# Kernel tuning notes

Measured on AMD Instinct MI355X. Metric: run time of the kernel, lower is better.

Reference implementation:

```python
import jax, jax.numpy as jnp
import numpy as np


def reference(x, weight, bias):
    """Per-sample dynamic conv2d, expressed as one grouped convolution.

    x:      (B, C_in, H, W)
    weight: (B, C_out, C_in, kH, kW)
    bias:   (B, C_out)
    returns (B, C_out, H_out, W_out) with H_out = H - kH + 1 (valid conv)
    """
    B, C_in, H, W = x.shape
    C_out, kH, kW = weight.shape[1], weight.shape[3], weight.shape[4]
    # Fold batch into channels: groups=B grouped conv == B independent convs.
    x_g = x.reshape(1, B * C_in, H, W)
    w_g = weight.reshape(B * C_out, C_in, kH, kW)
    out = jax.lax.conv_general_dilated(
        x_g, w_g,
        window_strides=(1, 1),
        padding='VALID',
        dimension_numbers=('NCHW', 'OIHW', 'NCHW'),
        feature_group_count=B,
    )  # (1, B*C_out, H_out, W_out)
    out = out.reshape(B, C_out, out.shape[2], out.shape[3])
    return out + bias[:, :, None, None]


def setup_inputs() -> dict:
    key = jax.random.key(0)
    k1, k2, k3 = jax.random.split(key, 3)
    B, C_in, C_out, H, W, kH, kW = 16, 64, 64, 128, 128, 3, 3
    x = jax.random.normal(k1, (B, C_in, H, W), dtype=jnp.float32)
    weight = jax.random.normal(k2, (B, C_out, C_in, kH, kW), dtype=jnp.float32) * 0.05
    bias = jax.random.normal(k3, (B, C_out), dtype=jnp.float32)
    return {"x": x, "weight": weight, "bias": bias}
```

## Files before the change

kernel.cpp:

```cpp
#include <hip/hip_runtime.h>
#include <hip/hip_bf16.h>

#define BATCH 16
#define CI 64
#define CO 64
#define H 128
#define W 128
#define HO 126
#define WO 126
#define HW (H * W)

typedef short bfrag __attribute__((ext_vector_type(8)));
typedef float ffrag __attribute__((ext_vector_type(4)));

static __device__ __forceinline__ unsigned short f2bf(float f) {
    unsigned u = __float_as_uint(f);
    u += 0x7fffu + ((u >> 16) & 1u);
    return (unsigned short)(u >> 16);
}

__global__ void wt_prepass(const float* __restrict__ w, unsigned short* __restrict__ w_t) {
    int i = blockIdx.x * 256 + threadIdx.x;
    int ci = i & 63;
    int co = (i >> 6) & 63;
    int bs = i >> 12;
    int b = bs / 9, s = bs - b * 9;
    w_t[i] = f2bf(w[(((b * 64 + co) * 64 + ci) * 9) + s]);
}

static __device__ __forceinline__ void stage_write(unsigned short* __restrict__ slabp,
                                                   const float4* __restrict__ v,
                                                   int st_o, int st_cg) {
    #pragma unroll
    for (int k = 0; k < 4; ++k) {
        const int col = st_cg * 4 + k;
        unsigned int u[4];
        #pragma unroll
        for (int e = 0; e < 4; ++e) {
            __hip_bfloat162 h2 = __float22bfloat162_rn(make_float2(
                ((const float*)&v[2 * e])[k], ((const float*)&v[2 * e + 1])[k]));
            u[e] = *(unsigned int*)&h2;
        }
        *(uint4*)&slabp[(col * 8 + (st_o ^ (col & 7))) * 8] = *(const uint4*)u;
    }
}

__launch_bounds__(256, 2)
__global__ void dynconv_fused(const float* __restrict__ x,
                              const unsigned short* __restrict__ w_t,
                              const float* __restrict__ bias,
                              float* __restrict__ out) {
    __shared__ __align__(16) unsigned short xs[4 * 8192];

    const int tid = threadIdx.x;
    const int gx  = blockIdx.x;
    const int b   = blockIdx.y;
    const int y0  = gx * 4;
    const int nunits = (gx == 31) ? 2 : 4;

    const int wave = tid >> 6, lane = tid & 63;
    const int l16 = lane & 15, lq = lane >> 4;

    const int st_o  = tid & 7;
    const int st_cg = tid >> 3;

    const float* stp = x + (size_t)b * CI * HW + (size_t)(st_o * 8) * HW + st_cg * 4;

    const bfrag* wtb = (const bfrag*)w_t + (size_t)(b * 9) * 512;
    const int co_b = wave * 16 + l16;
    bfrag a[9][2];
    #pragma unroll
    for (int s = 0; s < 9; ++s)
        #pragma unroll
        for (int ks = 0; ks < 2; ++ks)
            a[s][ks] = wtb[s * 512 + co_b * 8 + ks * 4 + lq];

    float bv[4];
    #pragma unroll
    for (int r = 0; r < 4; ++r)
        bv[r] = bias[b * 64 + wave * 16 + lq * 4 + r];

    {
        float4 v[3][8];
        #pragma unroll
        for (int rr = 0; rr < 3; ++rr) {
            const float* p = stp + (size_t)(y0 + rr) * W;
            #pragma unroll
            for (int e = 0; e < 8; ++e) v[rr][e] = *(const float4*)(p + (size_t)e * HW);
        }
        #pragma unroll
        for (int rr = 0; rr < 3; ++rr)
            stage_write(&xs[rr * 8192], v[rr], st_o, st_cg);
    }
    asm volatile("s_waitcnt lgkmcnt(0)" ::: "memory");
    __builtin_amdgcn_s_barrier();
    __builtin_amdgcn_sched_barrier(0);

    for (int j = 0; j < nunits; ++j) {
        const bool hn = (j + 1) < nunits;

        float4 v[8];
        if (hn) {
            const float* p = stp + (size_t)(y0 + j + 3) * W;
            #pragma unroll
            for (int e = 0; e < 8; ++e) v[e] = *(const float4*)(p + (size_t)e * HW);
        }
        __builtin_amdgcn_sched_barrier(0);

        ffrag acc[8];
        #pragma unroll
        for (int nt = 0; nt < 8; ++nt) acc[nt] = (ffrag){0.f, 0.f, 0.f, 0.f};

        #pragma unroll
        for (int s = 0; s < 9; ++s) {
            const int dy = s / 3, dx = s - dy * 3;
            const unsigned short* slabp = &xs[((j + dy) & 3) * 8192];
            #pragma unroll
            for (int ks = 0; ks < 2; ++ks) {
                const int o = ks * 4 + lq;
                #pragma unroll
                for (int nt = 0; nt < 8; ++nt) {
                    int colx = nt * 16 + l16 + dx;
                    if (colx > 127) colx = 127;
                    const bfrag bf = *(const bfrag*)&slabp[(colx * 8 + (o ^ (colx & 7))) * 8];
                    acc[nt] = __builtin_amdgcn_mfma_f32_16x16x32_bf16(a[s][ks], bf, acc[nt], 0, 0, 0);
                }
            }
        }

        if (hn) {
            stage_write(&xs[((j + 3) & 3) * 8192], v, st_o, st_cg);
            asm volatile("s_waitcnt lgkmcnt(0)" ::: "memory");
            __builtin_amdgcn_s_barrier();
            __builtin_amdgcn_sched_barrier(0);
        }

        const int oy = y0 + j;
        #pragma unroll
        for (int r = 0; r < 4; ++r) {
            float* op = out + ((size_t)(b * 64 + wave * 16 + lq * 4 + r) * HO + oy) * WO;
            const float bvv = bv[r];
            #pragma unroll
            for (int nt = 0; nt < 8; ++nt) {
                const int ox = nt * 16 + l16;
                if (ox < WO) op[ox] = acc[nt][r] + bvv;
            }
        }
    }
}

extern "C" void kernel_launch(void* const* d_in, const int* in_sizes, int n_in,
                              void* d_out, int out_size, void* d_ws, size_t ws_size,
                              hipStream_t stream) {
    const float* x    = (const float*)d_in[0];
    const float* w    = (const float*)d_in[1];
    const float* bias = (const float*)d_in[2];
    float* out        = (float*)d_out;

    unsigned short* w_t = (unsigned short*)d_ws;

    wt_prepass<<<dim3(589824 / 256), dim3(256), 0, stream>>>(w, w_t);
    dynconv_fused<<<dim3(32, BATCH), dim3(256), 0, stream>>>(x, w_t, bias, out);
}
```

Before: 134.2 us.

## Deepen input row prefetch to two rows ahead with five-slot LDS ring

Prefetches input rows two units ahead into alternating register buffers (vA/vB) and grows the LDS ring from four to five slabs. The loop is manually unrolled by two so the register buffers swap roles. This gives global loads a full extra unit of compute to hide their latency. It costs more registers (16 float4 held live) and more LDS, 80KB per block, which could reduce occupancy below the two blocks per CU requested by launch bounds.

```diff
diff --git a/kernel.cpp b/kernel.cpp
--- a/kernel.cpp
+++ b/kernel.cpp
@@ -50,7 +50,7 @@
                               const unsigned short* __restrict__ w_t,
                               const float* __restrict__ bias,
                               float* __restrict__ out) {
-    __shared__ __align__(16) unsigned short xs[4 * 8192];
+    __shared__ __align__(16) unsigned short xs[5 * 8192];
 
     const int tid = threadIdx.x;
     const int gx  = blockIdx.x;
@@ -80,6 +80,8 @@
     for (int r = 0; r < 4; ++r)
         bv[r] = bias[b * 64 + wave * 16 + lq * 4 + r];
 
+    float4 vA[8], vB[8];
+
     {
         float4 v[3][8];
         #pragma unroll
@@ -87,6 +89,11 @@
             const float* p = stp + (size_t)(y0 + rr) * W;
             #pragma unroll
             for (int e = 0; e < 8; ++e) v[rr][e] = *(const float4*)(p + (size_t)e * HW);
+        }
+        {
+            const float* p = stp + (size_t)(y0 + 3) * W;
+            #pragma unroll
+            for (int e = 0; e < 8; ++e) vA[e] = *(const float4*)(p + (size_t)e * HW);
         }
         #pragma unroll
         for (int rr = 0; rr < 3; ++rr)
@@ -96,57 +103,55 @@
     __builtin_amdgcn_s_barrier();
     __builtin_amdgcn_sched_barrier(0);
 
-    for (int j = 0; j < nunits; ++j) {
-        const bool hn = (j + 1) < nunits;
+#define UNIT(J_, VCUR, VNEXT)                                                   \
+    do {                                                                        \
+        const int jj = (J_);                                                    \
+        if (jj + 3 <= nunits) {                                                 \
+            const float* p = stp + (size_t)(y0 + jj + 4) * W;                   \
+            _Pragma("unroll") for (int e = 0; e < 8; ++e)                       \
+                VNEXT[e] = *(const float4*)(p + (size_t)e * HW);                \
+        }                                                                       \
+        __builtin_amdgcn_sched_barrier(0);                                      \
+        ffrag acc[8];                                                           \
+        _Pragma("unroll") for (int nt = 0; nt < 8; ++nt)                        \
+            acc[nt] = (ffrag){0.f, 0.f, 0.f, 0.f};                              \
+        _Pragma("unroll") for (int s = 0; s < 9; ++s) {                         \
+            const int dy = s / 3, dx = s - dy * 3;                              \
+            int t = jj + dy; if (t >= 5) t -= 5;                                \
+            const unsigned short* slabp = &xs[t * 8192];                        \
+            _Pragma("unroll") for (int ks = 0; ks < 2; ++ks) {                  \
+                const int o = ks * 4 + lq;                                      \
+                _Pragma("unroll") for (int nt = 0; nt < 8; ++nt) {              \
+                    int colx = nt * 16 + l16 + dx;                              \
+                    if (colx > 127) colx = 127;                                 \
+                    const bfrag bf = *(const bfrag*)&slabp[(colx * 8 + (o ^ (colx & 7))) * 8]; \
+                    acc[nt] = __builtin_amdgcn_mfma_f32_16x16x32_bf16(a[s][ks], bf, acc[nt], 0, 0, 0); \
+                }                                                               \
+            }                                                                   \
+        }                                                                       \
+        if (jj + 2 <= nunits) {                                                 \
+            int tw = jj + 3; if (tw >= 5) tw -= 5;                              \
+            stage_write(&xs[tw * 8192], VCUR, st_o, st_cg);                     \
+            asm volatile("s_waitcnt lgkmcnt(0)" ::: "memory");                  \
+            __builtin_amdgcn_s_barrier();                                       \
+            __builtin_amdgcn_sched_barrier(0);                                  \
+        }                                                                       \
+        const int oy = y0 + jj;                                                 \
+        _Pragma("unroll") for (int r = 0; r < 4; ++r) {                         \
+            float* op = out + ((size_t)(b * 64 + wave * 16 + lq * 4 + r) * HO + oy) * WO; \
+            const float bvv = bv[r];                                            \
+            _Pragma("unroll") for (int nt = 0; nt < 8; ++nt) {                  \
+                const int ox = nt * 16 + l16;                                   \
+                if (ox < WO) op[ox] = acc[nt][r] + bvv;                         \
+            }                                                                   \
+        }                                                                       \
+    } while (0)
 
-        float4 v[8];
-        if (hn) {
-            const float* p = stp + (size_t)(y0 + j + 3) * W;
-            #pragma unroll
-            for (int e = 0; e < 8; ++e) v[e] = *(const float4*)(p + (size_t)e * HW);
-        }
-        __builtin_amdgcn_sched_barrier(0);
-
-        ffrag acc[8];
-        #pragma unroll
-        for (int nt = 0; nt < 8; ++nt) acc[nt] = (ffrag){0.f, 0.f, 0.f, 0.f};
-
-        #pragma unroll
-        for (int s = 0; s < 9; ++s) {
-            const int dy = s / 3, dx = s - dy * 3;
-            const unsigned short* slabp = &xs[((j + dy) & 3) * 8192];
-            #pragma unroll
-            for (int ks = 0; ks < 2; ++ks) {
-                const int o = ks * 4 + lq;
-                #pragma unroll
-                for (int nt = 0; nt < 8; ++nt) {
-                    int colx = nt * 16 + l16 + dx;
-                    if (colx > 127) colx = 127;
-                    const bfrag bf = *(const bfrag*)&slabp[(colx * 8 + (o ^ (colx & 7))) * 8];
-                    acc[nt] = __builtin_amdgcn_mfma_f32_16x16x32_bf16(a[s][ks], bf, acc[nt], 0, 0, 0);
-                }
-            }
-        }
-
-        if (hn) {
-            stage_write(&xs[((j + 3) & 3) * 8192], v, st_o, st_cg);
-            asm volatile("s_waitcnt lgkmcnt(0)" ::: "memory");
-            __builtin_amdgcn_s_barrier();
-            __builtin_amdgcn_sched_barrier(0);
-        }
-
-        const int oy = y0 + j;
-        #pragma unroll
-        for (int r = 0; r < 4; ++r) {
-            float* op = out + ((size_t)(b * 64 + wave * 16 + lq * 4 + r) * HO + oy) * WO;
-            const float bvv = bv[r];
-            #pragma unroll
-            for (int nt = 0; nt < 8; ++nt) {
-                const int ox = nt * 16 + l16;
-                if (ox < WO) op[ox] = acc[nt][r] + bvv;
-            }
-        }
+    for (int j = 0; j < nunits; j += 2) {
+        UNIT(j, vA, vB);
+        UNIT(j + 1, vB, vA);
     }
+#undef UNIT
 }
 
 extern "C" void kernel_launch(void* const* d_in, const int* in_sizes, int n_in,
```

Result: slower. 155.6 us (+16.0%).

## Prepass x into swizzled bf16 rows and stage via async global_load_lds ring

Applied to the files above, without the earlier changes.

Adds a prepass kernel that converts x to bf16 in the swizzled LDS layout the conv kernel expects, one 16KB block per image row. The main kernel then copies rows straight into a 5-slot LDS ring with global_load_lds, prefetching rows ahead and waiting with vmcnt instead of staging through registers with conversion. This drops register-side conversion from the main loop and halves the bytes it reads. In exchange it adds an extra launch with a full read of x and a write of the bf16 copy, uses more LDS, and removes the occupancy hint of 2 blocks per CU.

```diff
diff --git a/kernel.cpp b/kernel.cpp
--- a/kernel.cpp
+++ b/kernel.cpp
@@ -12,6 +12,9 @@
 
 typedef short bfrag __attribute__((ext_vector_type(8)));
 typedef float ffrag __attribute__((ext_vector_type(4)));
+
+typedef __attribute__((address_space(1))) const unsigned char g_byte;
+typedef __attribute__((address_space(3))) unsigned char l_byte;
 
 static __device__ __forceinline__ unsigned short f2bf(float f) {
     unsigned u = __float_as_uint(f);
@@ -28,43 +31,54 @@
     w_t[i] = f2bf(w[(((b * 64 + co) * 64 + ci) * 9) + s]);
 }
 
-static __device__ __forceinline__ void stage_write(unsigned short* __restrict__ slabp,
-                                                   const float4* __restrict__ v,
-                                                   int st_o, int st_cg) {
+__global__ void xt_prepass(const float* __restrict__ x, unsigned short* __restrict__ x_t) {
+    __shared__ __align__(16) float lf[64 * 132];
+    const int row = blockIdx.x, b = blockIdx.y, t = threadIdx.x;
+
+    const float* xb = x + (size_t)b * CI * HW + (size_t)row * W;
+    {
+        const int ci0 = t >> 5, c4 = (t & 31) * 4;
+        #pragma unroll
+        for (int p = 0; p < 8; ++p) {
+            const int ci = p * 8 + ci0;
+            float4 v = *(const float4*)(xb + (size_t)ci * HW + c4);
+            *(float4*)&lf[ci * 132 + c4] = v;
+        }
+    }
+    __syncthreads();
+    unsigned short* xrow = x_t + ((size_t)(b * 128) + row) * 8192;
     #pragma unroll
-    for (int k = 0; k < 4; ++k) {
-        const int col = st_cg * 4 + k;
+    for (int cc = 0; cc < 4; ++cc) {
+        const int c = cc * 256 + t;
+        const int col = c >> 3, s8 = c & 7, o = s8 ^ (col & 7);
         unsigned int u[4];
         #pragma unroll
         for (int e = 0; e < 4; ++e) {
-            __hip_bfloat162 h2 = __float22bfloat162_rn(make_float2(
-                ((const float*)&v[2 * e])[k], ((const float*)&v[2 * e + 1])[k]));
+            float f0 = lf[(o * 8 + 2 * e) * 132 + col];
+            float f1 = lf[(o * 8 + 2 * e + 1) * 132 + col];
+            __hip_bfloat162 h2 = __float22bfloat162_rn(make_float2(f0, f1));
             u[e] = *(unsigned int*)&h2;
         }
-        *(uint4*)&slabp[(col * 8 + (st_o ^ (col & 7))) * 8] = *(const uint4*)u;
+        *(uint4*)&xrow[(size_t)c * 8] = *(const uint4*)u;
     }
 }
 
-__launch_bounds__(256, 2)
-__global__ void dynconv_fused(const float* __restrict__ x,
+__launch_bounds__(256)
+__global__ void dynconv_fused(const unsigned short* __restrict__ x_t,
                               const unsigned short* __restrict__ w_t,
                               const float* __restrict__ bias,
                               float* __restrict__ out) {
-    __shared__ __align__(16) unsigned short xs[4 * 8192];
+    __shared__ __align__(16) unsigned short xs[5 * 8192];
 
     const int tid = threadIdx.x;
     const int gx  = blockIdx.x;
     const int b   = blockIdx.y;
     const int y0  = gx * 4;
-    const int nunits = (gx == 31) ? 2 : 4;
+    const int nu  = (gx == 31) ? 2 : 4;
+    const int rmaxl = nu + 1;
 
     const int wave = tid >> 6, lane = tid & 63;
     const int l16 = lane & 15, lq = lane >> 4;
-
-    const int st_o  = tid & 7;
-    const int st_cg = tid >> 3;
-
-    const float* stp = x + (size_t)b * CI * HW + (size_t)(st_o * 8) * HW + st_cg * 4;
 
     const bfrag* wtb = (const bfrag*)w_t + (size_t)(b * 9) * 512;
     const int co_b = wave * 16 + l16;
@@ -80,33 +94,28 @@
     for (int r = 0; r < 4; ++r)
         bv[r] = bias[b * 64 + wave * 16 + lq * 4 + r];
 
-    {
-        float4 v[3][8];
-        #pragma unroll
-        for (int rr = 0; rr < 3; ++rr) {
-            const float* p = stp + (size_t)(y0 + rr) * W;
-            #pragma unroll
-            for (int e = 0; e < 8; ++e) v[rr][e] = *(const float4*)(p + (size_t)e * HW);
-        }
-        #pragma unroll
-        for (int rr = 0; rr < 3; ++rr)
-            stage_write(&xs[rr * 8192], v[rr], st_o, st_cg);
+    const unsigned short* xtb = x_t + ((size_t)(b * 128) + y0) * 8192;
+    const int lnoff = wave * 4096 + lane * 16;
+
+#define STAGE_ROW(RL, SL)                                                       \
+    do {                                                                        \
+        const char* gsrc_ = (const char*)(xtb + (size_t)(RL) * 8192) + lnoff;   \
+        l_byte* ldst_ = (l_byte*)((char*)&xs[(SL) * 8192] + wave * 4096);       \
+        _Pragma("unroll") for (int q_ = 0; q_ < 4; ++q_)                        \
+            __builtin_amdgcn_global_load_lds((g_byte*)(gsrc_ + q_ * 1024),      \
+                                             ldst_ + q_ * 1024, 16, 0, 0);      \
+    } while (0)
+
+    #pragma unroll
+    for (int r = 0; r < 5; ++r) {
+        const int rl = (r <= rmaxl) ? r : rmaxl;
+        STAGE_ROW(rl, r);
     }
-    asm volatile("s_waitcnt lgkmcnt(0)" ::: "memory");
+    asm volatile("s_waitcnt vmcnt(8)" ::: "memory");
     __builtin_amdgcn_s_barrier();
     __builtin_amdgcn_sched_barrier(0);
 
-    for (int j = 0; j < nunits; ++j) {
-        const bool hn = (j + 1) < nunits;
-
-        float4 v[8];
-        if (hn) {
-            const float* p = stp + (size_t)(y0 + j + 3) * W;
-            #pragma unroll
-            for (int e = 0; e < 8; ++e) v[e] = *(const float4*)(p + (size_t)e * HW);
-        }
-        __builtin_amdgcn_sched_barrier(0);
-
+    for (int j = 0; j < nu; ++j) {
         ffrag acc[8];
         #pragma unroll
         for (int nt = 0; nt < 8; ++nt) acc[nt] = (ffrag){0.f, 0.f, 0.f, 0.f};
@@ -114,7 +123,8 @@
         #pragma unroll
         for (int s = 0; s < 9; ++s) {
             const int dy = s / 3, dx = s - dy * 3;
-            const unsigned short* slabp = &xs[((j + dy) & 3) * 8192];
+            int t = j + dy; if (t >= 5) t -= 5;
+            const unsigned short* slabp = &xs[t * 8192];
             #pragma unroll
             for (int ks = 0; ks < 2; ++ks) {
                 const int o = ks * 4 + lq;
@@ -128,12 +138,20 @@
             }
         }
 
-        if (hn) {
-            stage_write(&xs[((j + 3) & 3) * 8192], v, st_o, st_cg);
-            asm volatile("s_waitcnt lgkmcnt(0)" ::: "memory");
-            __builtin_amdgcn_s_barrier();
-            __builtin_amdgcn_sched_barrier(0);
+        asm volatile("s_waitcnt lgkmcnt(0)" ::: "memory");
+        __builtin_amdgcn_s_barrier();
+        __builtin_amdgcn_sched_barrier(0);
+
+        {
+            const int rl = (j + 5 <= rmaxl) ? (j + 5) : rmaxl;
+            STAGE_ROW(rl, j);
         }
+        __builtin_amdgcn_sched_barrier(0);
+
+        if (j == 0) { asm volatile("s_waitcnt vmcnt(8)"  ::: "memory"); }
+        else        { asm volatile("s_waitcnt vmcnt(36)" ::: "memory"); }
+        __builtin_amdgcn_s_barrier();
+        __builtin_amdgcn_sched_barrier(0);
 
         const int oy = y0 + j;
         #pragma unroll
@@ -147,6 +165,7 @@
             }
         }
     }
+#undef STAGE_ROW
 }
 
 extern "C" void kernel_launch(void* const* d_in, const int* in_sizes, int n_in,
@@ -158,7 +177,9 @@
     float* out        = (float*)d_out;
 
     unsigned short* w_t = (unsigned short*)d_ws;
+    unsigned short* x_t = (unsigned short*)((char*)d_ws + 1179648);
 
     wt_prepass<<<dim3(589824 / 256), dim3(256), 0, stream>>>(w, w_t);
-    dynconv_fused<<<dim3(32, BATCH), dim3(256), 0, stream>>>(x, w_t, bias, out);
+    xt_prepass<<<dim3(128, BATCH), dim3(256), 0, stream>>>(x, x_t);
+    dynconv_fused<<<dim3(32, BATCH), dim3(256), 0, stream>>>(x_t, w_t, bias, out);
 }
```

Measured after the change: 146.9 us. 1.1x slower.
